# Kernel tuning notes

Hardware: AMD Instinct MI355X
Metric: run time of the kernel (lower is better)

## Reference

```python
import jax, jax.numpy as jnp
import numpy as np

BN_EPS = 1e-5


def mesh_conv(x, gemm, W):
    # x: [B, C, E], gemm: [B, E, 4] neighbor edge indices, W: [O, C, 5]
    # gather the 4 neighbor edge features per edge (per batch element)
    nbr = jax.vmap(lambda xb, gb: xb[:, gb])(x, gemm)  # [B, C, E, 4]
    f1, f2, f3, f4 = nbr[..., 0], nbr[..., 1], nbr[..., 2], nbr[..., 3]
    # MeshCNN symmetric functions over opposite neighbors
    f = jnp.stack(
        [x, f1 + f3, f2 + f4, jnp.abs(f1 - f3), jnp.abs(f2 - f4)], axis=-1
    )  # [B, C, E, 5]
    # Conv2d(in, out, kernel=(1,5), bias=False) == contraction over (C, 5)
    return jnp.einsum('bcek,ock->boe', f, W)  # [B, O, E]


def batchnorm_relu(x, gamma, beta):
    # BatchNorm2d in training mode (stats over batch and edge dims), applied
    # to relu(x) as in the original: bn(F.relu(x)); x is [B, C, E]
    h = jax.nn.relu(x)
    mean = jnp.mean(h, axis=(0, 2), keepdims=True)
    var = jnp.var(h, axis=(0, 2), keepdims=True)
    h = (h - mean) * jax.lax.rsqrt(var + BN_EPS)
    return h * gamma[None, :, None] + beta[None, :, None]


def setup_inputs() -> dict:
    key = jax.random.key(0)
    ks = jax.random.split(key, 5)
    B, C_in, C_out, E = 4, 128, 256, 30000
    x = jax.random.normal(ks[0], (B, C_in, E), dtype=jnp.float32)
    gemm = jax.random.randint(ks[1], (B, E, 4), 0, E, dtype=jnp.int32)
    W0 = jax.random.normal(ks[2], (C_out, C_in, 5), dtype=jnp.float32) * (1.0 / np.sqrt(C_in * 5))
    gamma1 = jnp.ones((C_out,), dtype=jnp.float32)
    beta1 = jnp.zeros((C_out,), dtype=jnp.float32)
    W1 = jax.random.normal(ks[3], (C_out, C_out, 5), dtype=jnp.float32) * (1.0 / np.sqrt(C_out * 5))
    return {"x": x, "gemm": gemm, "W0": W0, "gamma1": gamma1, "beta1": beta1, "W1": W1}


def reference(x, gemm, W0, gamma1, beta1, W1):
    x = mesh_conv(x, gemm, W0)          # conv0
    x1 = x                               # residual branch
    x = batchnorm_relu(x, gamma1, beta1)  # bn1(relu(x))
    x = mesh_conv(x, gemm, W1)          # conv1
    x = x + x1                           # residual add
    return jax.nn.relu(x)                # [B, C_out, E]
```

## Files before the change

### kernel.cpp

```cpp
#include <hip/hip_runtime.h>
#include <hip/hip_bf16.h>
#include <stdint.h>


#define BB 4
#define CIN 128
#define COUT 256
#define EE 30000
#define BN 64
#define NTILES 469
#define BC 64
#define KCH 320
#define PITCH 328
#define NBLK (NTILES * BB)
#define GRID1 1880

typedef __attribute__((ext_vector_type(8))) short bf16x8;
typedef __attribute__((ext_vector_type(4))) float f32x4;

static __device__ __forceinline__ float blo(unsigned u) {
    union { unsigned u; float f; } v; v.u = u << 16; return v.f;
}
static __device__ __forceinline__ float bhi(unsigned u) {
    union { unsigned u; float f; } v; v.u = u & 0xffff0000u; return v.f;
}
static __device__ __forceinline__ unsigned pk2(float lo, float hi) {
    __hip_bfloat162 h = __float22bfloat162_rn(float2{lo, hi});
    union { __hip_bfloat162 h; unsigned u; } v; v.h = h; return v.u;
}
static __device__ __forceinline__ unsigned short bf1(float f) {
    __hip_bfloat16 h = __float2bfloat16(f);
    union { __hip_bfloat16 h; unsigned short u; } v; v.h = h; return v.u;
}

__global__ __launch_bounds__(256) void k_transpose(const float* __restrict__ x,
                                                   unsigned short* __restrict__ xT) {
    __shared__ float tile[64][CIN + 1];
    const int t = threadIdx.x;
    const int e0 = blockIdx.x * 64;
    const int b = blockIdx.y;
    const int el = t & 63;
    const bool ok = (e0 + el) < EE;
    const float* xb = x + (size_t)b * CIN * EE;
#pragma unroll
    for (int cc = 0; cc < CIN / 4; ++cc) {
        const int c = cc * 4 + (t >> 6);
        tile[el][c] = ok ? xb[(size_t)c * EE + e0 + el] : 0.f;
    }
    __syncthreads();
    const int el2 = t >> 2, cq = t & 3;
    if (e0 + el2 < EE) {
        unsigned ov[16];
#pragma unroll
        for (int i = 0; i < 16; ++i)
            ov[i] = pk2(tile[el2][cq * 32 + 2 * i], tile[el2][cq * 32 + 2 * i + 1]);
        int4* dst = (int4*)(xT + ((size_t)b * EE + e0 + el2) * CIN + cq * 32);
#pragma unroll
        for (int j = 0; j < 4; ++j)
            dst[j] = make_int4((int)ov[4 * j], (int)ov[4 * j + 1], (int)ov[4 * j + 2], (int)ov[4 * j + 3]);
    }
}

__global__ __launch_bounds__(256) void k_wprep(const float* __restrict__ W,
                                               unsigned short* __restrict__ Wf,
                                               const float* __restrict__ ss,
                                               int C, int K) {
    const int id = blockIdx.x * 256 + threadIdx.x;
    if (id >= 256 * K) return;
    const int m = id / K;
    const int G = id % K;
    const int chunk = G / KCH;
    const int r = G % KCH;
    const int k = r / BC;
    const int c = chunk * BC + (r % BC);
    float val = W[((size_t)m * C + c) * 5 + k];
    if (ss) {
        const float sc = ss[c];
        val *= (k < 3) ? sc : fabsf(sc);
    }
    Wf[((size_t)(G / 32) * 256 + m) * 32 + (G % 32)] = bf1(val);
}

__global__ __launch_bounds__(256) void k_stats(const float* __restrict__ partials,
                                               const float* __restrict__ gamma,
                                               const float* __restrict__ beta,
                                               float* __restrict__ ss) {
    const int ch = blockIdx.x;
    const int t = threadIdx.x;
    float s = 0.f, q = 0.f;
    for (int i = t; i < NBLK; i += 256) {
        s += partials[(size_t)i * 512 + ch];
        q += partials[(size_t)i * 512 + 256 + ch];
    }
    __shared__ float ls[256], lq[256];
    ls[t] = s; lq[t] = q;
    __syncthreads();
    for (int off = 128; off > 0; off >>= 1) {
        if (t < off) { ls[t] += ls[t + off]; lq[t] += lq[t + off]; }
        __syncthreads();
    }
    if (t == 0) {
        const float inv = 1.f / (float)(BB * EE);
        const float mean = ls[0] * inv;
        const float var = lq[0] * inv - mean * mean;
        const float sc = gamma[ch] * rsqrtf(var + 1e-5f);
        ss[ch] = sc;
        ss[COUT + ch] = beta[ch] - mean * sc;
    }
}

__global__ __launch_bounds__(256) void k_bias(const float* __restrict__ W1,
                                              const float* __restrict__ ss,
                                              float* __restrict__ bias) {
    const int o = blockIdx.x, t = threadIdx.x;
    const float sh = ss[COUT + t];
    const float* wr = W1 + ((size_t)o * COUT + t) * 5;
    float v = sh * (wr[0] + 2.f * (wr[1] + wr[2]));
    __shared__ float red[256];
    red[t] = v;
    __syncthreads();
    for (int off = 128; off > 0; off >>= 1) {
        if (t < off) red[t] += red[t + off];
        __syncthreads();
    }
    if (t == 0) bias[o] = red[0];
}

template <int C, int CHUNKS, int IS1>
__global__ __launch_bounds__(256, 2) void k_conv(
    const unsigned short* __restrict__ xin,
    const int* __restrict__ gmm,
    const unsigned short* __restrict__ Wf,
    const float* __restrict__ bias,
    unsigned short* __restrict__ x1,
    unsigned short* __restrict__ rT,
    float* __restrict__ partials,
    float* __restrict__ out) {
    __shared__ unsigned short f_lds[64 * PITCH];
    const int t = threadIdx.x;
    const int w = t >> 6, lane = t & 63;
    const int ml = lane & 15, g = lane >> 4;
    const int i = blockIdx.x;
    const int b = (i & 7) >> 1;
    const int tile = ((i >> 3) << 1) | (i & 1);
    if (tile >= NTILES) return;
    const int e0 = tile * BN;

    const int be = t >> 2, bq = t & 3;
    const int eb = e0 + be;
    const int ec = (eb < EE) ? eb : 0;
    const int4 nb = *(const int4*)(gmm + ((size_t)b * EE + ec) * 4);

    const unsigned short* xb = xin + (size_t)b * EE * C;
    const unsigned short* rowc = xb + (size_t)ec * C;
    const unsigned short* row1 = xb + (size_t)nb.x * C;
    const unsigned short* row2 = xb + (size_t)nb.y * C;
    const unsigned short* row3 = xb + (size_t)nb.z * C;
    const unsigned short* row4 = xb + (size_t)nb.w * C;

    f32x4 acc[4][4];
#pragma unroll
    for (int ii = 0; ii < 4; ++ii)
#pragma unroll
        for (int jj = 0; jj < 4; ++jj)
            acc[ii][jj] = (f32x4){0.f, 0.f, 0.f, 0.f};

    int4 bufA[10], bufB[10];

    auto stage = [&](int chunk, int4* dst) {
        const int cb = chunk * BC + bq * 16;
        dst[0] = *(const int4*)(row1 + cb); dst[1] = *(const int4*)(row1 + cb + 8);
        dst[2] = *(const int4*)(row3 + cb); dst[3] = *(const int4*)(row3 + cb + 8);
        dst[4] = *(const int4*)(row2 + cb); dst[5] = *(const int4*)(row2 + cb + 8);
        dst[6] = *(const int4*)(row4 + cb); dst[7] = *(const int4*)(row4 + cb + 8);
        dst[8] = *(const int4*)(rowc + cb); dst[9] = *(const int4*)(rowc + cb + 8);
    };

    auto step = [&](int chunk, const int4* cur, int4* nxt, bool donext) {
        if (donext) stage(chunk + 1, nxt);

        const unsigned* u13a = (const unsigned*)&cur[0];
        const unsigned* u13b = (const unsigned*)&cur[2];
        const unsigned* u24a = (const unsigned*)&cur[4];
        const unsigned* u24b = (const unsigned*)&cur[6];
        const unsigned* uc   = (const unsigned*)&cur[8];
        unsigned o1[8], o2[8], o3[8], o4[8];
#pragma unroll
        for (int j = 0; j < 8; ++j) {
            const float a0 = blo(u13a[j]), a1 = bhi(u13a[j]);
            const float b0 = blo(u13b[j]), b1 = bhi(u13b[j]);
            o1[j] = pk2(a0 + b0, a1 + b1);
            o3[j] = pk2(fabsf(a0 - b0), fabsf(a1 - b1));
        }
#pragma unroll
        for (int j = 0; j < 8; ++j) {
            const float a0 = blo(u24a[j]), a1 = bhi(u24a[j]);
            const float b0 = blo(u24b[j]), b1 = bhi(u24b[j]);
            o2[j] = pk2(a0 + b0, a1 + b1);
            o4[j] = pk2(fabsf(a0 - b0), fabsf(a1 - b1));
        }

        __syncthreads();
        {
            unsigned short* bp = &f_lds[be * PITCH + bq * 16];
            *(int4*)(bp + 0 * BC)     = make_int4((int)uc[0], (int)uc[1], (int)uc[2], (int)uc[3]);
            *(int4*)(bp + 0 * BC + 8) = make_int4((int)uc[4], (int)uc[5], (int)uc[6], (int)uc[7]);
            *(int4*)(bp + 1 * BC)     = make_int4((int)o1[0], (int)o1[1], (int)o1[2], (int)o1[3]);
            *(int4*)(bp + 1 * BC + 8) = make_int4((int)o1[4], (int)o1[5], (int)o1[6], (int)o1[7]);
            *(int4*)(bp + 2 * BC)     = make_int4((int)o2[0], (int)o2[1], (int)o2[2], (int)o2[3]);
            *(int4*)(bp + 2 * BC + 8) = make_int4((int)o2[4], (int)o2[5], (int)o2[6], (int)o2[7]);
            *(int4*)(bp + 3 * BC)     = make_int4((int)o3[0], (int)o3[1], (int)o3[2], (int)o3[3]);
            *(int4*)(bp + 3 * BC + 8) = make_int4((int)o3[4], (int)o3[5], (int)o3[6], (int)o3[7]);
            *(int4*)(bp + 4 * BC)     = make_int4((int)o4[0], (int)o4[1], (int)o4[2], (int)o4[3]);
            *(int4*)(bp + 4 * BC + 8) = make_int4((int)o4[4], (int)o4[5], (int)o4[6], (int)o4[7]);
        }
        __syncthreads();

        const unsigned short* wp = Wf + (size_t)chunk * (KCH / 32) * COUT * 32;
#pragma unroll 2
        for (int kk = 0; kk < KCH / 32; ++kk) {
            union { int4 i; bf16x8 h; } af[4], bfr[4];
#pragma unroll
            for (int fm = 0; fm < 4; ++fm)
                af[fm].i = *(const int4*)(wp + ((size_t)kk * COUT + (w * 64 + fm * 16 + ml)) * 32 + g * 8);
#pragma unroll
            for (int fn = 0; fn < 4; ++fn)
                bfr[fn].i = *(const int4*)&f_lds[(fn * 16 + ml) * PITCH + kk * 32 + g * 8];
#pragma unroll
            for (int fm = 0; fm < 4; ++fm)
#pragma unroll
                for (int fn = 0; fn < 4; ++fn)
                    acc[fm][fn] = __builtin_amdgcn_mfma_f32_16x16x32_bf16(af[fm].h, bfr[fn].h, acc[fm][fn], 0, 0, 0);
        }
    };

    stage(0, bufA);
#pragma unroll 1
    for (int cp = 0; cp < CHUNKS / 2; ++cp) {
        step(2 * cp, bufA, bufB, true);
        step(2 * cp + 1, bufB, bufA, (2 * cp + 2) < CHUNKS);
    }

    const size_t fragbase = (((size_t)b * NTILES + tile) * 4 + w) * 16;
    if (!IS1) {
        float ks[4][4], kq[4][4];
#pragma unroll
        for (int fm = 0; fm < 4; ++fm)
#pragma unroll
            for (int r = 0; r < 4; ++r) { ks[fm][r] = 0.f; kq[fm][r] = 0.f; }
#pragma unroll
        for (int fm = 0; fm < 4; ++fm) {
#pragma unroll
            for (int fn = 0; fn < 4; ++fn) {
                const int fi = fm * 4 + fn;
                uint2 pk;
                pk.x = pk2(acc[fm][fn][0], acc[fm][fn][1]);
                pk.y = pk2(acc[fm][fn][2], acc[fm][fn][3]);
                *(uint2*)(x1 + (fragbase + fi) * 256 + lane * 4) = pk;
                const int e = e0 + fn * 16 + ml;
                float rv0 = fmaxf(acc[fm][fn][0], 0.f), rv1 = fmaxf(acc[fm][fn][1], 0.f);
                float rv2 = fmaxf(acc[fm][fn][2], 0.f), rv3 = fmaxf(acc[fm][fn][3], 0.f);
                if (e < EE) {
                    uint2 pr;
                    pr.x = pk2(rv0, rv1);
                    pr.y = pk2(rv2, rv3);
                    *(uint2*)(rT + ((size_t)b * EE + e) * COUT + w * 64 + fm * 16 + g * 4) = pr;
                } else {
                    rv0 = rv1 = rv2 = rv3 = 0.f;
                }
                ks[fm][0] += rv0; kq[fm][0] += rv0 * rv0;
                ks[fm][1] += rv1; kq[fm][1] += rv1 * rv1;
                ks[fm][2] += rv2; kq[fm][2] += rv2 * rv2;
                ks[fm][3] += rv3; kq[fm][3] += rv3 * rv3;
            }
        }
#pragma unroll
        for (int fm = 0; fm < 4; ++fm) {
#pragma unroll
            for (int r = 0; r < 4; ++r) {
#pragma unroll
                for (int m = 1; m < 16; m <<= 1) {
                    ks[fm][r] += __shfl_xor(ks[fm][r], m);
                    kq[fm][r] += __shfl_xor(kq[fm][r], m);
                }
            }
        }
        if (ml == 0) {
            float* pp = partials + ((size_t)b * NTILES + tile) * 512;
#pragma unroll
            for (int fm = 0; fm < 4; ++fm) {
                const int ch = w * 64 + fm * 16 + g * 4;
                *(float4*)(pp + ch)       = make_float4(ks[fm][0], ks[fm][1], ks[fm][2], ks[fm][3]);
                *(float4*)(pp + 256 + ch) = make_float4(kq[fm][0], kq[fm][1], kq[fm][2], kq[fm][3]);
            }
        }
    } else {
#pragma unroll
        for (int fm = 0; fm < 4; ++fm) {
            const int chb = w * 64 + fm * 16 + g * 4;
            const float4 bv = *(const float4*)(bias + chb);
#pragma unroll
            for (int fn = 0; fn < 4; ++fn) {
                const int fi = fm * 4 + fn;
                const uint2 pk = *(const uint2*)(x1 + (fragbase + fi) * 256 + lane * 4);
                const int e = e0 + fn * 16 + ml;
                if (e < EE) {
                    float* op = out + ((size_t)b * COUT + chb) * EE + e;
                    op[0]              = fmaxf(acc[fm][fn][0] + bv.x + blo(pk.x), 0.f);
                    op[(size_t)EE]     = fmaxf(acc[fm][fn][1] + bv.y + bhi(pk.x), 0.f);
                    op[(size_t)2 * EE] = fmaxf(acc[fm][fn][2] + bv.z + blo(pk.y), 0.f);
                    op[(size_t)3 * EE] = fmaxf(acc[fm][fn][3] + bv.w + bhi(pk.y), 0.f);
                }
            }
        }
    }
}

extern "C" void kernel_launch(void* const* d_in, const int* in_sizes, int n_in,
                              void* d_out, int out_size, void* d_ws, size_t ws_size,
                              hipStream_t stream) {
    const float* x = (const float*)d_in[0];
    const int* gmm = (const int*)d_in[1];
    const float* W0 = (const float*)d_in[2];
    const float* gamma = (const float*)d_in[3];
    const float* beta = (const float*)d_in[4];
    const float* W1 = (const float*)d_in[5];
    float* out = (float*)d_out;

    char* ws = (char*)d_ws;
    unsigned short* xT  = (unsigned short*)(ws);
    unsigned short* Wf0 = (unsigned short*)(ws + 30720000);
    unsigned short* Wf1 = (unsigned short*)(ws + 31047680);
    unsigned short* x1  = (unsigned short*)(ws + 31703040);
    unsigned short* rT  = (unsigned short*)(ws + 93175808);
    float* partials     = (float*)(ws + 154615808);
    float* ss           = (float*)(ws + 158457856);
    float* bias         = (float*)(ws + 158459904);

    k_transpose<<<dim3(NTILES, BB), 256, 0, stream>>>(x, xT);
    k_wprep<<<dim3(640), 256, 0, stream>>>(W0, Wf0, nullptr, CIN, 640);
    k_conv<CIN, 2, 0><<<dim3(GRID1), 256, 0, stream>>>(
        xT, gmm, Wf0, nullptr, x1, rT, partials, nullptr);
    k_stats<<<dim3(256), 256, 0, stream>>>(partials, gamma, beta, ss);
    k_bias<<<dim3(256), 256, 0, stream>>>(W1, ss, bias);
    k_wprep<<<dim3(1280), 256, 0, stream>>>(W1, Wf1, ss, COUT, 1280);
    k_conv<COUT, 4, 1><<<dim3(GRID1), 256, 0, stream>>>(
        rT, gmm, Wf1, bias, x1, nullptr, nullptr, out);
}
```

Baseline: 478.2 us.

## Use 512-thread conv blocks with 8 waves splitting edge tile and channels

Each conv block now has 512 threads (8 waves) instead of 256. Waves split the 64-edge tile into two halves on top of the four channel groups, so each wave keeps a 4x2 accumulator grid instead of 4x4. The gather stage is reshaped so each thread loads 8 channels instead of 16. The register double-buffer is replaced by a single buffer whose next-chunk prefetch is issued between the LDS write and the barrier. The LDS pitch changes, and the partial-stats layout doubles, with per-half entries reduced in k_stats. The aim is more waves for latency hiding and lower register pressure, at the cost of less prefetch overlap and reloading each weight fragment in both edge-half waves.

```diff
diff --git a/kernel.cpp b/kernel.cpp
--- a/kernel.cpp
+++ b/kernel.cpp
@@ -11,7 +11,7 @@
 #define NTILES 469
 #define BC 64
 #define KCH 320
-#define PITCH 328
+#define PITCH 344
 #define NBLK (NTILES * BB)
 #define GRID1 1880
 
@@ -88,7 +88,7 @@
     const int ch = blockIdx.x;
     const int t = threadIdx.x;
     float s = 0.f, q = 0.f;
-    for (int i = t; i < NBLK; i += 256) {
+    for (int i = t; i < NBLK * 2; i += 256) {
         s += partials[(size_t)i * 512 + ch];
         q += partials[(size_t)i * 512 + 256 + ch];
     }
@@ -127,7 +127,7 @@
 }
 
 template <int C, int CHUNKS, int IS1>
-__global__ __launch_bounds__(256, 2) void k_conv(
+__global__ __launch_bounds__(512, 4) void k_conv(
     const unsigned short* __restrict__ xin,
     const int* __restrict__ gmm,
     const unsigned short* __restrict__ Wf,
@@ -140,13 +140,14 @@
     const int t = threadIdx.x;
     const int w = t >> 6, lane = t & 63;
     const int ml = lane & 15, g = lane >> 4;
+    const int wch = w & 3, weh = w >> 2;
     const int i = blockIdx.x;
     const int b = (i & 7) >> 1;
     const int tile = ((i >> 3) << 1) | (i & 1);
     if (tile >= NTILES) return;
     const int e0 = tile * BN;
 
-    const int be = t >> 2, bq = t & 3;
+    const int be = t >> 3, bq = t & 7;
     const int eb = e0 + be;
     const int ec = (eb < EE) ? eb : 0;
     const int4 nb = *(const int4*)(gmm + ((size_t)b * EE + ec) * 4);
@@ -158,90 +159,79 @@
     const unsigned short* row3 = xb + (size_t)nb.z * C;
     const unsigned short* row4 = xb + (size_t)nb.w * C;
 
-    f32x4 acc[4][4];
+    f32x4 acc[4][2];
 #pragma unroll
     for (int ii = 0; ii < 4; ++ii)
 #pragma unroll
-        for (int jj = 0; jj < 4; ++jj)
+        for (int jj = 0; jj < 2; ++jj)
             acc[ii][jj] = (f32x4){0.f, 0.f, 0.f, 0.f};
 
-    int4 bufA[10], bufB[10];
-
-    auto stage = [&](int chunk, int4* dst) {
-        const int cb = chunk * BC + bq * 16;
-        dst[0] = *(const int4*)(row1 + cb); dst[1] = *(const int4*)(row1 + cb + 8);
-        dst[2] = *(const int4*)(row3 + cb); dst[3] = *(const int4*)(row3 + cb + 8);
-        dst[4] = *(const int4*)(row2 + cb); dst[5] = *(const int4*)(row2 + cb + 8);
-        dst[6] = *(const int4*)(row4 + cb); dst[7] = *(const int4*)(row4 + cb + 8);
-        dst[8] = *(const int4*)(rowc + cb); dst[9] = *(const int4*)(rowc + cb + 8);
+    int4 buf[5];
+
+    auto stage = [&](int chunk) {
+        const int cb = chunk * BC + bq * 8;
+        buf[0] = *(const int4*)(row1 + cb);
+        buf[1] = *(const int4*)(row3 + cb);
+        buf[2] = *(const int4*)(row2 + cb);
+        buf[3] = *(const int4*)(row4 + cb);
+        buf[4] = *(const int4*)(rowc + cb);
     };
 
-    auto step = [&](int chunk, const int4* cur, int4* nxt, bool donext) {
-        if (donext) stage(chunk + 1, nxt);
-
-        const unsigned* u13a = (const unsigned*)&cur[0];
-        const unsigned* u13b = (const unsigned*)&cur[2];
-        const unsigned* u24a = (const unsigned*)&cur[4];
-        const unsigned* u24b = (const unsigned*)&cur[6];
-        const unsigned* uc   = (const unsigned*)&cur[8];
-        unsigned o1[8], o2[8], o3[8], o4[8];
-#pragma unroll
-        for (int j = 0; j < 8; ++j) {
-            const float a0 = blo(u13a[j]), a1 = bhi(u13a[j]);
-            const float b0 = blo(u13b[j]), b1 = bhi(u13b[j]);
+    stage(0);
+#pragma unroll 1
+    for (int chunk = 0; chunk < CHUNKS; ++chunk) {
+        const unsigned* r1 = (const unsigned*)&buf[0];
+        const unsigned* r3 = (const unsigned*)&buf[1];
+        const unsigned* r2 = (const unsigned*)&buf[2];
+        const unsigned* r4 = (const unsigned*)&buf[3];
+        const int4 ctr = buf[4];
+        unsigned o1[4], o2[4], o3[4], o4[4];
+#pragma unroll
+        for (int j = 0; j < 4; ++j) {
+            const float a0 = blo(r1[j]), a1 = bhi(r1[j]);
+            const float b0 = blo(r3[j]), b1 = bhi(r3[j]);
             o1[j] = pk2(a0 + b0, a1 + b1);
             o3[j] = pk2(fabsf(a0 - b0), fabsf(a1 - b1));
         }
 #pragma unroll
-        for (int j = 0; j < 8; ++j) {
-            const float a0 = blo(u24a[j]), a1 = bhi(u24a[j]);
-            const float b0 = blo(u24b[j]), b1 = bhi(u24b[j]);
+        for (int j = 0; j < 4; ++j) {
+            const float a0 = blo(r2[j]), a1 = bhi(r2[j]);
+            const float b0 = blo(r4[j]), b1 = bhi(r4[j]);
             o2[j] = pk2(a0 + b0, a1 + b1);
             o4[j] = pk2(fabsf(a0 - b0), fabsf(a1 - b1));
         }
 
         __syncthreads();
         {
-            unsigned short* bp = &f_lds[be * PITCH + bq * 16];
-            *(int4*)(bp + 0 * BC)     = make_int4((int)uc[0], (int)uc[1], (int)uc[2], (int)uc[3]);
-            *(int4*)(bp + 0 * BC + 8) = make_int4((int)uc[4], (int)uc[5], (int)uc[6], (int)uc[7]);
-            *(int4*)(bp + 1 * BC)     = make_int4((int)o1[0], (int)o1[1], (int)o1[2], (int)o1[3]);
-            *(int4*)(bp + 1 * BC + 8) = make_int4((int)o1[4], (int)o1[5], (int)o1[6], (int)o1[7]);
-            *(int4*)(bp + 2 * BC)     = make_int4((int)o2[0], (int)o2[1], (int)o2[2], (int)o2[3]);
-            *(int4*)(bp + 2 * BC + 8) = make_int4((int)o2[4], (int)o2[5], (int)o2[6], (int)o2[7]);
-            *(int4*)(bp + 3 * BC)     = make_int4((int)o3[0], (int)o3[1], (int)o3[2], (int)o3[3]);
-            *(int4*)(bp + 3 * BC + 8) = make_int4((int)o3[4], (int)o3[5], (int)o3[6], (int)o3[7]);
-            *(int4*)(bp + 4 * BC)     = make_int4((int)o4[0], (int)o4[1], (int)o4[2], (int)o4[3]);
-            *(int4*)(bp + 4 * BC + 8) = make_int4((int)o4[4], (int)o4[5], (int)o4[6], (int)o4[7]);
-        }
+            unsigned short* bp = &f_lds[be * PITCH + bq * 8];
+            *(int4*)(bp + 0 * BC) = ctr;
+            *(int4*)(bp + 1 * BC) = make_int4((int)o1[0], (int)o1[1], (int)o1[2], (int)o1[3]);
+            *(int4*)(bp + 2 * BC) = make_int4((int)o2[0], (int)o2[1], (int)o2[2], (int)o2[3]);
+            *(int4*)(bp + 3 * BC) = make_int4((int)o3[0], (int)o3[1], (int)o3[2], (int)o3[3]);
+            *(int4*)(bp + 4 * BC) = make_int4((int)o4[0], (int)o4[1], (int)o4[2], (int)o4[3]);
+        }
+        if (chunk + 1 < CHUNKS) stage(chunk + 1);
         __syncthreads();
 
         const unsigned short* wp = Wf + (size_t)chunk * (KCH / 32) * COUT * 32;
 #pragma unroll 2
         for (int kk = 0; kk < KCH / 32; ++kk) {
-            union { int4 i; bf16x8 h; } af[4], bfr[4];
+            union { int4 i; bf16x8 h; } af[4], bfr[2];
 #pragma unroll
             for (int fm = 0; fm < 4; ++fm)
-                af[fm].i = *(const int4*)(wp + ((size_t)kk * COUT + (w * 64 + fm * 16 + ml)) * 32 + g * 8);
-#pragma unroll
-            for (int fn = 0; fn < 4; ++fn)
-                bfr[fn].i = *(const int4*)&f_lds[(fn * 16 + ml) * PITCH + kk * 32 + g * 8];
+                af[fm].i = *(const int4*)(wp + ((size_t)kk * COUT + (wch * 64 + fm * 16 + ml)) * 32 + g * 8);
+#pragma unroll
+            for (int fn = 0; fn < 2; ++fn)
+                bfr[fn].i = *(const int4*)&f_lds[(weh * 32 + fn * 16 + ml) * PITCH + kk * 32 + g * 8];
 #pragma unroll
             for (int fm = 0; fm < 4; ++fm)
 #pragma unroll
-                for (int fn = 0; fn < 4; ++fn)
+                for (int fn = 0; fn < 2; ++fn)
                     acc[fm][fn] = __builtin_amdgcn_mfma_f32_16x16x32_bf16(af[fm].h, bfr[fn].h, acc[fm][fn], 0, 0, 0);
         }
-    };
-
-    stage(0, bufA);
-#pragma unroll 1
-    for (int cp = 0; cp < CHUNKS / 2; ++cp) {
-        step(2 * cp, bufA, bufB, true);
-        step(2 * cp + 1, bufB, bufA, (2 * cp + 2) < CHUNKS);
-    }
-
-    const size_t fragbase = (((size_t)b * NTILES + tile) * 4 + w) * 16;
+    }
+
+    const size_t fragbase = (((size_t)(b * NTILES + tile)) * 8 + w) * 8;
     if (!IS1) {
         float ks[4][4], kq[4][4];
 #pragma unroll
@@ -251,20 +241,20 @@
 #pragma unroll
         for (int fm = 0; fm < 4; ++fm) {
 #pragma unroll
-            for (int fn = 0; fn < 4; ++fn) {
-                const int fi = fm * 4 + fn;
+            for (int fn = 0; fn < 2; ++fn) {
+                const int fi = fm * 2 + fn;
                 uint2 pk;
                 pk.x = pk2(acc[fm][fn][0], acc[fm][fn][1]);
                 pk.y = pk2(acc[fm][fn][2], acc[fm][fn][3]);
                 *(uint2*)(x1 + (fragbase + fi) * 256 + lane * 4) = pk;
-                const int e = e0 + fn * 16 + ml;
+                const int e = e0 + weh * 32 + fn * 16 + ml;
                 float rv0 = fmaxf(acc[fm][fn][0], 0.f), rv1 = fmaxf(acc[fm][fn][1], 0.f);
                 float rv2 = fmaxf(acc[fm][fn][2], 0.f), rv3 = fmaxf(acc[fm][fn][3], 0.f);
                 if (e < EE) {
                     uint2 pr;
                     pr.x = pk2(rv0, rv1);
                     pr.y = pk2(rv2, rv3);
-                    *(uint2*)(rT + ((size_t)b * EE + e) * COUT + w * 64 + fm * 16 + g * 4) = pr;
+                    *(uint2*)(rT + ((size_t)b * EE + e) * COUT + wch * 64 + fm * 16 + g * 4) = pr;
                 } else {
                     rv0 = rv1 = rv2 = rv3 = 0.f;
                 }
@@ -286,10 +276,10 @@
             }
         }
         if (ml == 0) {
-            float* pp = partials + ((size_t)b * NTILES + tile) * 512;
+            float* pp = partials + ((size_t)(b * NTILES + tile) * 2 + weh) * 512;
 #pragma unroll
             for (int fm = 0; fm < 4; ++fm) {
-                const int ch = w * 64 + fm * 16 + g * 4;
+                const int ch = wch * 64 + fm * 16 + g * 4;
                 *(float4*)(pp + ch)       = make_float4(ks[fm][0], ks[fm][1], ks[fm][2], ks[fm][3]);
                 *(float4*)(pp + 256 + ch) = make_float4(kq[fm][0], kq[fm][1], kq[fm][2], kq[fm][3]);
             }
@@ -297,13 +287,13 @@
     } else {
 #pragma unroll
         for (int fm = 0; fm < 4; ++fm) {
-            const int chb = w * 64 + fm * 16 + g * 4;
+            const int chb = wch * 64 + fm * 16 + g * 4;
             const float4 bv = *(const float4*)(bias + chb);
 #pragma unroll
-            for (int fn = 0; fn < 4; ++fn) {
-                const int fi = fm * 4 + fn;
+            for (int fn = 0; fn < 2; ++fn) {
+                const int fi = fm * 2 + fn;
                 const uint2 pk = *(const uint2*)(x1 + (fragbase + fi) * 256 + lane * 4);
-                const int e = e0 + fn * 16 + ml;
+                const int e = e0 + weh * 32 + fn * 16 + ml;
                 if (e < EE) {
                     float* op = out + ((size_t)b * COUT + chb) * EE + e;
                     op[0]              = fmaxf(acc[fm][fn][0] + bv.x + blo(pk.x), 0.f);
@@ -334,16 +324,16 @@
     unsigned short* x1  = (unsigned short*)(ws + 31703040);
     unsigned short* rT  = (unsigned short*)(ws + 93175808);
     float* partials     = (float*)(ws + 154615808);
-    float* ss           = (float*)(ws + 158457856);
-    float* bias         = (float*)(ws + 158459904);
+    float* ss           = (float*)(ws + 162299904);
+    float* bias         = (float*)(ws + 162301952);
 
     k_transpose<<<dim3(NTILES, BB), 256, 0, stream>>>(x, xT);
     k_wprep<<<dim3(640), 256, 0, stream>>>(W0, Wf0, nullptr, CIN, 640);
-    k_conv<CIN, 2, 0><<<dim3(GRID1), 256, 0, stream>>>(
+    k_conv<CIN, 2, 0><<<dim3(GRID1), 512, 0, stream>>>(
         xT, gmm, Wf0, nullptr, x1, rT, partials, nullptr);
     k_stats<<<dim3(256), 256, 0, stream>>>(partials, gamma, beta, ss);
     k_bias<<<dim3(256), 256, 0, stream>>>(W1, ss, bias);
     k_wprep<<<dim3(1280), 256, 0, stream>>>(W1, Wf1, ss, COUT, 1280);
-    k_conv<COUT, 4, 1><<<dim3(GRID1), 256, 0, stream>>>(
+    k_conv<COUT, 4, 1><<<dim3(GRID1), 512, 0, stream>>>(
         rT, gmm, Wf1, bias, x1, nullptr, nullptr, out);
 }
```

New measurement: 542.6 us. 13.5% more time.
